# Optimization experiments

Measured on AMD Instinct MI355X. Metric: run time of the kernel, lower is better.

The kernel has to match this reference:

```python
import jax, jax.numpy as jnp
import numpy as np

N = 10000       # nodes (cells)
NFEAT = 2000    # gene-expression features
NFE = 256       # embed features
NH = 128        # nhid
NHE = 64        # nhid_embed
L = 2           # gcn_hid_layers_num
NOUT = 20       # output classes
BN_EPS = 1e-5


def bn_eval(x, g, b, rm, rv):
    # BatchNorm1d in eval mode: affine with running stats
    return g * (x - rm) / jnp.sqrt(rv + BN_EPS) + b


def lstm_layer(seq, Wih, Whh, bih, bhh):
    # seq: [T, N, H_in]; PyTorch gate order i, f, g, o
    Hd = Whh.shape[1]
    def step(carry, xt):
        h, c = carry
        z = xt @ Wih.T + h @ Whh.T + bih + bhh  # [N, 4H]
        i, f, g, o = jnp.split(z, 4, axis=1)
        c = jax.nn.sigmoid(f) * c + jax.nn.sigmoid(i) * jnp.tanh(g)
        h = jax.nn.sigmoid(o) * jnp.tanh(c)
        return (h, c), h
    h0 = jnp.zeros((seq.shape[1], Hd), seq.dtype)
    _, hs = jax.lax.scan(step, (h0, h0), seq)
    return hs  # [T, N, H]


def setup_inputs() -> dict:
    key = jax.random.key(0)
    ks = iter(jax.random.split(key, 48))
    def rn(shape, scale=1.0):
        return jax.random.normal(next(ks), shape, dtype=jnp.float32) * scale
    inp = {}
    inp["x"] = rn((N, NFEAT))
    inp["embed"] = rn((N, NFE))
    inp["adj"] = jax.random.uniform(next(ks), (N, N), dtype=jnp.float32)
    inp["W_in"] = rn((NH, NFEAT), NFEAT ** -0.5); inp["b_in"] = jnp.zeros((NH,), jnp.float32)
    inp["bn_in_g"] = jnp.ones((NH,), jnp.float32); inp["bn_in_b"] = jnp.zeros((NH,), jnp.float32)
    inp["bn_in_rm"] = rn((NH,), 0.1); inp["bn_in_rv"] = jnp.ones((NH,), jnp.float32)
    # gs_block: Linear(2*nhid -> nhid) per layer (concat self + mean-aggregated neighbors)
    inp["W_gs"] = rn((L, NH, 2 * NH), (2 * NH) ** -0.5); inp["b_gs"] = jnp.zeros((L, NH), jnp.float32)
    for l in range(2):  # 2-layer LSTM jumping-knowledge
        inp[f"Wih{l}"] = rn((4 * NH, NH), NH ** -0.5)
        inp[f"Whh{l}"] = rn((4 * NH, NH), NH ** -0.5)
        inp[f"bih{l}"] = jnp.zeros((4 * NH,), jnp.float32)
        inp[f"bhh{l}"] = jnp.zeros((4 * NH,), jnp.float32)
    inp["W_emb"] = rn((NHE, NFE), NFE ** -0.5); inp["b_emb"] = jnp.zeros((NHE,), jnp.float32)
    inp["bn_emb_g"] = jnp.ones((NHE,), jnp.float32); inp["bn_emb_b"] = jnp.zeros((NHE,), jnp.float32)
    inp["bn_emb_rm"] = rn((NHE,), 0.1); inp["bn_emb_rv"] = jnp.ones((NHE,), jnp.float32)
    D = NH + NHE
    inp["W_fc"] = rn((D, D), D ** -0.5); inp["b_fc"] = jnp.zeros((D,), jnp.float32)
    inp["bn_fc_g"] = jnp.ones((D,), jnp.float32); inp["bn_fc_b"] = jnp.zeros((D,), jnp.float32)
    inp["bn_fc_rm"] = rn((D,), 0.1); inp["bn_fc_rv"] = jnp.ones((D,), jnp.float32)
    inp["W_out"] = rn((NOUT, D), D ** -0.5); inp["b_out"] = jnp.zeros((NOUT,), jnp.float32)
    return inp


def _forward(x, embed, adj, W_in, b_in, bn_in_g, bn_in_b, bn_in_rm, bn_in_rv,
             W_gs, b_gs, Wih0, Whh0, bih0, bhh0, Wih1, Whh1, bih1, bhh1,
             W_emb, b_emb, bn_emb_g, bn_emb_b, bn_emb_rm, bn_emb_rv,
             W_fc, b_fc, bn_fc_g, bn_fc_b, bn_fc_rm, bn_fc_rv, W_out, b_out):
    # input projection + BN + ELU (dropout: eval mode -> no-op)
    h = jax.nn.elu(bn_eval(x @ W_in.T + b_in, bn_in_g, bn_in_b, bn_in_rm, bn_in_rv))
    # GraphSAGE mean aggregator: row-normalized dense adjacency
    adj_norm = adj / adj.sum(1, keepdims=True)
    jk = []
    for l in range(L):
        neigh = adj_norm @ h                              # [N, NH] neighbor mean
        comb = jnp.concatenate([h, neigh], axis=1)        # [N, 2NH] (gcn=False)
        h = jax.nn.relu(comb @ W_gs[l].T + b_gs[l])
        h = h / jnp.maximum(jnp.linalg.norm(h, axis=1, keepdims=True), 1e-12)  # F.normalize
        jk.append(h)
    seq = jnp.stack(jk, 0)                                # [L, N, NH]
    hs = lstm_layer(seq, Wih0, Whh0, bih0, bhh0)
    hs = lstm_layer(hs, Wih1, Whh1, bih1, bhh1)
    h = hs.mean(0)                                        # JK: mean of LSTM outputs
    h = jax.nn.elu(bn_eval(h, bn_in_g, bn_in_b, bn_in_rm, bn_in_rv))  # bn_node_in_exp reused
    e = jax.nn.elu(bn_eval(embed @ W_emb.T + b_emb, bn_emb_g, bn_emb_b, bn_emb_rm, bn_emb_rv))
    h = jnp.concatenate([h, e], axis=1)                   # [N, NH+NHE]
    h = jax.nn.elu(bn_eval(h @ W_fc.T + b_fc, bn_fc_g, bn_fc_b, bn_fc_rm, bn_fc_rv))
    logits = h @ W_out.T + b_out
    return jax.nn.log_softmax(logits, axis=1)


def reference(x, embed, adj, W_in, b_in, bn_in_g, bn_in_b, bn_in_rm, bn_in_rv,
              W_gs, b_gs, Wih0, Whh0, bih0, bhh0, Wih1, Whh1, bih1, bhh1,
              W_emb, b_emb, bn_emb_g, bn_emb_b, bn_emb_rm, bn_emb_rv,
              W_fc, b_fc, bn_fc_g, bn_fc_b, bn_fc_rm, bn_fc_rv, W_out, b_out):
    return _forward(x, embed, adj, W_in, b_in, bn_in_g, bn_in_b, bn_in_rm, bn_in_rv,
                    W_gs, b_gs, Wih0, Whh0, bih0, bhh0, Wih1, Whh1, bih1, bhh1,
                    W_emb, b_emb, bn_emb_g, bn_emb_b, bn_emb_rm, bn_emb_rv,
                    W_fc, b_fc, bn_fc_g, bn_fc_b, bn_fc_rm, bn_fc_rv, W_out, b_out)
```

## Files before the change

### kernel.cpp

```cpp
#include <hip/hip_runtime.h>
#include <hip/hip_bf16.h>
#include <math.h>

#define N_NODES 10000
#define NFEAT   2000
#define NFE     256
#define NH      128
#define NHE     64
#define NOUT    20
#define DCAT    192
#define BN_EPS  1e-5f

#define KP      10016
#define KSTEPS  313
#define MT      157
#define NSPLIT  16
#define KC      20
#define NSPLX   4
#define MPAD    10048

typedef __attribute__((ext_vector_type(8))) short  bf16x8;
typedef __attribute__((ext_vector_type(4))) float  f32x4;

__device__ __forceinline__ float sigm(float x) { return 1.0f / (1.0f + expf(-x)); }

__device__ __forceinline__ unsigned short f2bf(float x) {
    union { __hip_bfloat16 h; unsigned short u; } c;
    c.h = __float2bfloat16(x);
    return c.u;
}

__device__ __forceinline__ float bf2f(unsigned short u) {
    union { float f; unsigned int i; } c;
    c.i = ((unsigned int)u) << 16;
    return c.f;
}

__device__ __forceinline__ bf16x8 cvt8(const float* v) {
    bf16x8 r;
    #pragma unroll
    for (int i = 0; i < 8; ++i) r[i] = (short)f2bf(v[i]);
    return r;
}

__global__ __launch_bounds__(256) void wconv_kernel(const float* __restrict__ Wih0,
                                                    const float* __restrict__ Whh0,
                                                    const float* __restrict__ Wih1,
                                                    const float* __restrict__ Whh1,
                                                    const float* __restrict__ Wgs,
                                                    unsigned short* __restrict__ wl,
                                                    unsigned short* __restrict__ wgb)
{
    const int total = 262144 + 65536;
    for (int i = blockIdx.x * 256 + threadIdx.x; i < total; i += gridDim.x * 256) {
        if (i < 262144) {
            int l = i >> 17, rem = i & 131071;
            int n = rem >> 8, k = rem & 255;
            const float* src;
            if (l == 0) src = (k < 128) ? (Wih0 + n * 128 + k) : (Whh0 + n * 128 + (k - 128));
            else        src = (k < 128) ? (Wih1 + n * 128 + k) : (Whh1 + n * 128 + (k - 128));
            wl[i] = f2bf(*src);
        } else {
            int j = i - 262144;
            wgb[j] = f2bf(Wgs[j]);
        }
    }
}

__global__ __launch_bounds__(256) void adjmm_kernel(const float* __restrict__ adj,
                                                    const unsigned short* __restrict__ hT,
                                                    unsigned short* __restrict__ part,
                                                    float* __restrict__ part_s)
{
    __shared__ unsigned short sa[2][64 * 32];
    __shared__ unsigned short sb[2][128 * 32];
    const int tid  = threadIdx.x;
    const int lane = tid & 63, w = tid >> 6;
    const int m0   = blockIdx.x * 64;
    const int ks0  = blockIdx.y * KC;
    const int ks1  = min(ks0 + KC, KSTEPS);
    const int r0   = (w & 1) * 32;
    const int c0   = (w >> 1) * 64;

    const int arow = tid >> 2, agrp = tid & 3;
    const size_t abase = (size_t)min(m0 + arow, N_NODES - 1) * N_NODES;
    const int bcol = tid >> 1, bg0 = (tid & 1) * 2;

    const int asoff  = arow * 32 + ((agrp ^ (arow & 3)) << 3);
    const int bsoff0 = bcol * 32 + (((bg0 + 0) ^ (bcol & 3)) << 3);
    const int bsoff1 = bcol * 32 + (((bg0 + 1) ^ (bcol & 3)) << 3);

    float rs = 0.f;
    f32x4 acc[2][4];
    #pragma unroll
    for (int i = 0; i < 2; ++i)
        #pragma unroll
        for (int j = 0; j < 4; ++j) acc[i][j] = (f32x4){0.f, 0.f, 0.f, 0.f};

    float av8[8];
    bf16x8 vb0, vb1;
    auto load_step = [&](int ks) {
        const int k0 = ks * 32;
        const int kg = k0 + agrp * 8;
        if (kg + 8 <= N_NODES) {
            float4 u0 = *(const float4*)(adj + abase + kg);
            float4 u1 = *(const float4*)(adj + abase + kg + 4);
            av8[0] = u0.x; av8[1] = u0.y; av8[2] = u0.z; av8[3] = u0.w;
            av8[4] = u1.x; av8[5] = u1.y; av8[6] = u1.z; av8[7] = u1.w;
        } else {
            #pragma unroll
            for (int i = 0; i < 8; ++i) av8[i] = 0.f;
        }
        vb0 = *(const bf16x8*)(hT + (size_t)bcol * KP + k0 + bg0 * 8);
        vb1 = *(const bf16x8*)(hT + (size_t)bcol * KP + k0 + (bg0 + 1) * 8);
    };
    auto write_step = [&](int p) {
        #pragma unroll
        for (int i = 0; i < 8; ++i) rs += av8[i];
        *(bf16x8*)(sa[p] + asoff)  = cvt8(av8);
        *(bf16x8*)(sb[p] + bsoff0) = vb0;
        *(bf16x8*)(sb[p] + bsoff1) = vb1;
    };

    load_step(ks0);
    write_step(0);

    for (int ks = ks0; ks < ks1; ++ks) {
        const int p = (ks - ks0) & 1;
        const bool more = (ks + 1 < ks1);
        if (more) load_step(ks + 1);
        __syncthreads();
        bf16x8 av[2], bv[4];
        #pragma unroll
        for (int rb = 0; rb < 2; ++rb) {
            int row = r0 + rb * 16 + (lane & 15);
            int g   = lane >> 4;
            av[rb] = *(const bf16x8*)(sa[p] + row * 32 + ((g ^ (row & 3)) << 3));
        }
        #pragma unroll
        for (int cb = 0; cb < 4; ++cb) {
            int col = c0 + cb * 16 + (lane & 15);
            int g   = lane >> 4;
            bv[cb] = *(const bf16x8*)(sb[p] + col * 32 + ((g ^ (col & 3)) << 3));
        }
        #pragma unroll
        for (int rb = 0; rb < 2; ++rb)
            #pragma unroll
            for (int cb = 0; cb < 4; ++cb)
                acc[rb][cb] = __builtin_amdgcn_mfma_f32_16x16x32_bf16(av[rb], bv[cb],
                                                                      acc[rb][cb], 0, 0, 0);
        if (more) write_step(p ^ 1);
    }

    rs += __shfl_xor(rs, 1);
    rs += __shfl_xor(rs, 2);
    if ((tid & 3) == 0) part_s[(size_t)blockIdx.y * MPAD + m0 + arow] = rs;

    unsigned short* pout = part + (size_t)blockIdx.y * MPAD * NH;
    #pragma unroll
    for (int rb = 0; rb < 2; ++rb)
        #pragma unroll
        for (int cb = 0; cb < 4; ++cb) {
            int rowb = m0 + r0 + rb * 16 + (lane >> 4) * 4;
            int col  = c0 + cb * 16 + (lane & 15);
            #pragma unroll
            for (int reg = 0; reg < 4; ++reg)
                pout[(size_t)(rowb + reg) * NH + col] = f2bf(acc[rb][cb][reg]);
        }
}

__global__ __launch_bounds__(256) void xw_mfma_kernel(const float* __restrict__ x,
                                                      const float* __restrict__ Wn,
                                                      float* __restrict__ part)
{
    __shared__ unsigned short sa[2][64 * 32];
    __shared__ unsigned short sb[2][128 * 32];
    const int tid  = threadIdx.x;
    const int lane = tid & 63, w = tid >> 6;
    const int m0   = blockIdx.x * 64;
    const int TOT  = (NFEAT + 31) / 32;
    const int s0   = blockIdx.y * 16;
    const int s1   = min(s0 + 16, TOT);
    const int r0   = (w & 1) * 32;
    const int c0   = (w >> 1) * 64;

    const int arow = tid >> 2, agrp = tid & 3;
    const size_t abase = (size_t)min(m0 + arow, N_NODES - 1) * NFEAT;
    const int asoff = arow * 32 + ((agrp ^ (arow & 3)) << 3);
    int bn_[2], bgrp_[2], bsoff_[2];
    #pragma unroll
    for (int t = 0; t < 2; ++t) {
        int gi = tid + t * 256;
        bn_[t] = gi >> 2; bgrp_[t] = gi & 3;
        bsoff_[t] = bn_[t] * 32 + ((bgrp_[t] ^ (bn_[t] & 3)) << 3);
    }

    f32x4 acc[2][4];
    #pragma unroll
    for (int i = 0; i < 2; ++i)
        #pragma unroll
        for (int j = 0; j < 4; ++j) acc[i][j] = (f32x4){0.f, 0.f, 0.f, 0.f};

    float av8[8], bv8[2][8];
    auto load_step = [&](int ks) {
        const int k0 = ks * 32;
        {
            const int kg = k0 + agrp * 8;
            if (kg + 8 <= NFEAT) {
                float4 u0 = *(const float4*)(x + abase + kg);
                float4 u1 = *(const float4*)(x + abase + kg + 4);
                av8[0]=u0.x; av8[1]=u0.y; av8[2]=u0.z; av8[3]=u0.w;
                av8[4]=u1.x; av8[5]=u1.y; av8[6]=u1.z; av8[7]=u1.w;
            } else {
                #pragma unroll
                for (int i = 0; i < 8; ++i) av8[i] = 0.f;
            }
        }
        #pragma unroll
        for (int t = 0; t < 2; ++t) {
            int kg = k0 + bgrp_[t] * 8;
            if (kg + 8 <= NFEAT) {
                float4 u0 = *(const float4*)(Wn + (size_t)bn_[t] * NFEAT + kg);
                float4 u1 = *(const float4*)(Wn + (size_t)bn_[t] * NFEAT + kg + 4);
                bv8[t][0]=u0.x; bv8[t][1]=u0.y; bv8[t][2]=u0.z; bv8[t][3]=u0.w;
                bv8[t][4]=u1.x; bv8[t][5]=u1.y; bv8[t][6]=u1.z; bv8[t][7]=u1.w;
            } else {
                #pragma unroll
                for (int i = 0; i < 8; ++i) bv8[t][i] = 0.f;
            }
        }
    };
    auto write_step = [&](int p) {
        *(bf16x8*)(sa[p] + asoff) = cvt8(av8);
        #pragma unroll
        for (int t = 0; t < 2; ++t)
            *(bf16x8*)(sb[p] + bsoff_[t]) = cvt8(bv8[t]);
    };

    load_step(s0);
    write_step(0);

    for (int ks = s0; ks < s1; ++ks) {
        const int p = (ks - s0) & 1;
        const bool more = (ks + 1 < s1);
        if (more) load_step(ks + 1);
        __syncthreads();
        bf16x8 av[2], bv[4];
        #pragma unroll
        for (int rb = 0; rb < 2; ++rb) {
            int row = r0 + rb * 16 + (lane & 15);
            int g   = lane >> 4;
            av[rb] = *(const bf16x8*)(sa[p] + row * 32 + ((g ^ (row & 3)) << 3));
        }
        #pragma unroll
        for (int cb = 0; cb < 4; ++cb) {
            int col = c0 + cb * 16 + (lane & 15);
            int g   = lane >> 4;
            bv[cb] = *(const bf16x8*)(sb[p] + col * 32 + ((g ^ (col & 3)) << 3));
        }
        #pragma unroll
        for (int rb = 0; rb < 2; ++rb)
            #pragma unroll
            for (int cb = 0; cb < 4; ++cb)
                acc[rb][cb] = __builtin_amdgcn_mfma_f32_16x16x32_bf16(av[rb], bv[cb],
                                                                      acc[rb][cb], 0, 0, 0);
        if (more) write_step(p ^ 1);
    }
    float* pout = part + (size_t)blockIdx.y * MPAD * NH;
    #pragma unroll
    for (int rb = 0; rb < 2; ++rb)
        #pragma unroll
        for (int cb = 0; cb < 4; ++cb) {
            int rowb = m0 + r0 + rb * 16 + (lane >> 4) * 4;
            int col  = c0 + cb * 16 + (lane & 15);
            #pragma unroll
            for (int reg = 0; reg < 4; ++reg)
                pout[(size_t)(rowb + reg) * NH + col] = acc[rb][cb][reg];
        }
}

__global__ __launch_bounds__(256) void xw_reduce_kernel(const float* __restrict__ part,
                                                        const float* __restrict__ bias,
                                                        const float* __restrict__ g,
                                                        const float* __restrict__ bb,
                                                        const float* __restrict__ rm,
                                                        const float* __restrict__ rv,
                                                        float* __restrict__ h,
                                                        unsigned short* __restrict__ hT)
{
    __shared__ unsigned short tb[128][8];
    const int tid = threadIdx.x;
    int idx = blockIdx.x * 256 + tid;
    const int c4 = (tid & 31) * 4;
    const int lr = tid >> 5;
    const int m0g = blockIdx.x * 8;
    const size_t ch = (size_t)MPAD * NH / 4;
    const float4* p = (const float4*)part;
    float a[4] = {0.f, 0.f, 0.f, 0.f};
    #pragma unroll
    for (int c = 0; c < NSPLX; ++c) {
        float4 v = p[c * ch + idx];
        a[0] += v.x; a[1] += v.y; a[2] += v.z; a[3] += v.w;
    }
    float o[4];
    #pragma unroll
    for (int j = 0; j < 4; ++j) {
        int c = c4 + j;
        float sc = g[c] / sqrtf(rv[c] + BN_EPS);
        float t = (a[j] + bias[c] - rm[c]) * sc + bb[c];
        o[j] = t > 0.f ? t : expm1f(t);
        tb[c][lr] = f2bf(o[j]);
    }
    float4 ov; ov.x = o[0]; ov.y = o[1]; ov.z = o[2]; ov.w = o[3];
    *(float4*)(h + (size_t)idx * 4) = ov;
    __syncthreads();
    if (tid < 128) {
        ushort4 v0, v1;
        v0.x = tb[tid][0]; v0.y = tb[tid][1]; v0.z = tb[tid][2]; v0.w = tb[tid][3];
        v1.x = tb[tid][4]; v1.y = tb[tid][5]; v1.z = tb[tid][6]; v1.w = tb[tid][7];
        *(ushort4*)(hT + (size_t)tid * KP + m0g)     = v0;
        *(ushort4*)(hT + (size_t)tid * KP + m0g + 4) = v1;
        if (blockIdx.x == 0) {
            ushort4 zz; zz.x = zz.y = zz.z = zz.w = 0;
            #pragma unroll
            for (int q = 0; q < 4; ++q)
                *(ushort4*)(hT + (size_t)tid * KP + 10000 + q * 4) = zz;
        }
    }
}

template<bool WRITE_T>
__global__ __launch_bounds__(256) void gs_fused_kernel(const float* __restrict__ h,
                                                       const unsigned short* __restrict__ part,
                                                       const float* __restrict__ part_s,
                                                       const unsigned short* __restrict__ Wg,
                                                       const float* __restrict__ bg,
                                                       float* __restrict__ jk,
                                                       unsigned short* __restrict__ jkT)
{
    __shared__ unsigned short sa[64 * 32];
    __shared__ unsigned short sb[128 * 32];
    __shared__ float ssq_l[64][2];
    __shared__ unsigned short tb[WRITE_T ? 128 * 64 : 1];
    const int tid  = threadIdx.x;
    const int lane = tid & 63, w = tid >> 6;
    const int m0   = blockIdx.x * 64;
    const int r0   = (w & 1) * 32;
    const int c0   = (w >> 1) * 64;
    const int arow = tid >> 2, agrp = tid & 3;
    const int mg   = min(m0 + arow, N_NODES - 1);

    float inv;
    {
        float s = 0.f;
        #pragma unroll
        for (int c = 0; c < NSPLIT; ++c) s += part_s[(size_t)c * MPAD + mg];
        inv = 1.0f / s;
    }

    f32x4 acc[2][4];
    #pragma unroll
    for (int i = 0; i < 2; ++i)
        #pragma unroll
        for (int j = 0; j < 4; ++j) acc[i][j] = (f32x4){0.f, 0.f, 0.f, 0.f};

    for (int k0 = 0; k0 < 256; k0 += 32) {
        const int kg = k0 + agrp * 8;
        float a8[8];
        if (kg < 128) {
            const float* asrc = h + (size_t)mg * NH + kg;
            float4 u0 = *(const float4*)asrc;
            float4 u1 = *(const float4*)(asrc + 4);
            a8[0]=u0.x; a8[1]=u0.y; a8[2]=u0.z; a8[3]=u0.w;
            a8[4]=u1.x; a8[5]=u1.y; a8[6]=u1.z; a8[7]=u1.w;
        } else {
            const int cc = kg - 128;
            float s[8] = {0.f,0.f,0.f,0.f,0.f,0.f,0.f,0.f};
            #pragma unroll
            for (int c = 0; c < NSPLIT; ++c) {
                bf16x8 v = *(const bf16x8*)(part + (size_t)c * MPAD * NH + (size_t)mg * NH + cc);
                #pragma unroll
                for (int i = 0; i < 8; ++i) s[i] += bf2f((unsigned short)v[i]);
            }
            #pragma unroll
            for (int i = 0; i < 8; ++i) a8[i] = s[i] * inv;
        }
        bf16x8 b8[2];
        #pragma unroll
        for (int t = 0; t < 2; ++t) {
            int gi = tid + t * 256;
            int n = gi >> 2, grp = gi & 3;
            b8[t] = *(const bf16x8*)(Wg + (size_t)n * 256 + k0 + grp * 8);
        }
        __syncthreads();
        *(bf16x8*)(sa + arow * 32 + ((agrp ^ (arow & 3)) << 3)) = cvt8(a8);
        #pragma unroll
        for (int t = 0; t < 2; ++t) {
            int gi = tid + t * 256;
            int n = gi >> 2, grp = gi & 3;
            *(bf16x8*)(sb + n * 32 + ((grp ^ (n & 3)) << 3)) = b8[t];
        }
        __syncthreads();
        bf16x8 av[2], bv[4];
        #pragma unroll
        for (int rb = 0; rb < 2; ++rb) {
            int row = r0 + rb * 16 + (lane & 15);
            int g   = lane >> 4;
            av[rb] = *(const bf16x8*)(sa + row * 32 + ((g ^ (row & 3)) << 3));
        }
        #pragma unroll
        for (int cb = 0; cb < 4; ++cb) {
            int col = c0 + cb * 16 + (lane & 15);
            int g   = lane >> 4;
            bv[cb] = *(const bf16x8*)(sb + col * 32 + ((g ^ (col & 3)) << 3));
        }
        #pragma unroll
        for (int rb = 0; rb < 2; ++rb)
            #pragma unroll
            for (int cb = 0; cb < 4; ++cb)
                acc[rb][cb] = __builtin_amdgcn_mfma_f32_16x16x32_bf16(av[rb], bv[cb],
                                                                      acc[rb][cb], 0, 0, 0);
    }

    float vv[2][4][4];
    float ps[2][4] = {};
    #pragma unroll
    for (int rb = 0; rb < 2; ++rb)
        #pragma unroll
        for (int cb = 0; cb < 4; ++cb) {
            int colg = c0 + cb * 16 + (lane & 15);
            float b = bg[colg];
            #pragma unroll
            for (int reg = 0; reg < 4; ++reg) {
                float t = fmaxf(acc[rb][cb][reg] + b, 0.f);
                vv[rb][cb][reg] = t;
                ps[rb][reg] += t * t;
            }
        }
    #pragma unroll
    for (int msk = 1; msk < 16; msk <<= 1)
        #pragma unroll
        for (int rb = 0; rb < 2; ++rb)
            #pragma unroll
            for (int reg = 0; reg < 4; ++reg)
                ps[rb][reg] += __shfl_xor(ps[rb][reg], msk);
    if ((lane & 15) == 0) {
        #pragma unroll
        for (int rb = 0; rb < 2; ++rb)
            #pragma unroll
            for (int reg = 0; reg < 4; ++reg)
                ssq_l[r0 + rb * 16 + (lane >> 4) * 4 + reg][w >> 1] = ps[rb][reg];
    }
    __syncthreads();
    #pragma unroll
    for (int rb = 0; rb < 2; ++rb)
        #pragma unroll
        for (int reg = 0; reg < 4; ++reg) {
            int lr = r0 + rb * 16 + (lane >> 4) * 4 + reg;
            float s = ssq_l[lr][0] + ssq_l[lr][1];
            float sc = 1.0f / fmaxf(sqrtf(s), 1e-12f);
            int m = m0 + lr;
            #pragma unroll
            for (int cb = 0; cb < 4; ++cb) {
                int colg = c0 + cb * 16 + (lane & 15);
                float o = vv[rb][cb][reg] * sc;
                if (m < N_NODES) jk[(size_t)m * NH + colg] = o;
                if constexpr (WRITE_T) tb[colg * 64 + lr] = f2bf(o);
            }
        }
    if constexpr (WRITE_T) {
        __syncthreads();
        #pragma unroll
        for (int p = 0; p < 4; ++p) {
            int flat = (tid + p * 256) * 8;
            int c = flat >> 6, mo = flat & 63;
            int kglob = m0 + mo;
            if (kglob < KP) {
                unsigned short tmp[8];
                #pragma unroll
                for (int i = 0; i < 8; ++i)
                    tmp[i] = (kglob + i < N_NODES) ? tb[c * 64 + mo + i] : (unsigned short)0;
                ushort4 v0, v1;
                v0.x = tmp[0]; v0.y = tmp[1]; v0.z = tmp[2]; v0.w = tmp[3];
                v1.x = tmp[4]; v1.y = tmp[5]; v1.z = tmp[6]; v1.w = tmp[7];
                *(ushort4*)(jkT + (size_t)c * KP + kglob)     = v0;
                *(ushort4*)(jkT + (size_t)c * KP + kglob + 4) = v1;
            }
        }
    }
}

__global__ __launch_bounds__(256) void lstm4_kernel(
    const float* __restrict__ jk0, const float* __restrict__ jk1,
    const unsigned short* __restrict__ wl,
    const float* __restrict__ bih0, const float* __restrict__ bhh0,
    const float* __restrict__ bih1, const float* __restrict__ bhh1,
    const float* __restrict__ bng, const float* __restrict__ bnb,
    const float* __restrict__ bnrm, const float* __restrict__ bnrv,
    float* __restrict__ hpost)
{
    __shared__ unsigned short sa[32 * 32];
    __shared__ unsigned short sb[512 * 32];
    __shared__ unsigned short hb[2][32][136];
    const int tid = threadIdx.x, lane = tid & 63, w = tid >> 6;
    const int m0 = blockIdx.x * 32;
    const int arow = tid >> 2, agrp = tid & 3;
    const int mg = min(m0 + arow, N_NODES - 1);

    f32x4 acc[2][8];
    float cst[2][2][4];

    auto zacc = [&] {
        #pragma unroll
        for (int i = 0; i < 2; ++i)
            #pragma unroll
            for (int j = 0; j < 8; ++j) acc[i][j] = (f32x4){0.f, 0.f, 0.f, 0.f};
    };
    auto stage_sb = [&](const unsigned short* wlayer, int k0) {
        #pragma unroll
        for (int t = 0; t < 8; ++t) {
            int gi = tid + t * 256, n = gi >> 2, grp = gi & 3;
            *(bf16x8*)(sb + n * 32 + ((grp ^ (n & 3)) << 3)) =
                *(const bf16x8*)(wlayer + (size_t)n * 256 + k0 + grp * 8);
        }
    };
    auto stage_sa = [&](const float* a, int k0) {
        if (tid < 128) {
            int kg = k0 + agrp * 8;
            const float* src = a + (size_t)mg * NH + kg;
            float4 u0 = *(const float4*)src, u1 = *(const float4*)(src + 4);
            float a8[8] = {u0.x, u0.y, u0.z, u0.w, u1.x, u1.y, u1.z, u1.w};
            *(bf16x8*)(sa + arow * 32 + ((agrp ^ (arow & 3)) << 3)) = cvt8(a8);
        }
    };
    auto av_sa = [&](int rb) {
        int row = rb * 16 + (lane & 15), g = lane >> 4;
        return *(const bf16x8*)(sa + row * 32 + ((g ^ (row & 3)) << 3));
    };
    auto av_hb = [&](int i, int rb, int kl) {
        int row = rb * 16 + (lane & 15), g = lane >> 4;
        return *(const bf16x8*)(&hb[i][row][kl + g * 8]);
    };
    auto mfma_all = [&](bf16x8 a0, bf16x8 a1) {
        #pragma unroll
        for (int gate = 0; gate < 4; ++gate)
            #pragma unroll
            for (int cb = 0; cb < 2; ++cb) {
                int col = gate * 128 + w * 32 + cb * 16 + (lane & 15);
                int g = lane >> 4;
                bf16x8 bv = *(const bf16x8*)(sb + col * 32 + ((g ^ (col & 3)) << 3));
                acc[0][gate * 2 + cb] =
                    __builtin_amdgcn_mfma_f32_16x16x32_bf16(a0, bv, acc[0][gate * 2 + cb], 0, 0, 0);
                acc[1][gate * 2 + cb] =
                    __builtin_amdgcn_mfma_f32_16x16x32_bf16(a1, bv, acc[1][gate * 2 + cb], 0, 0, 0);
            }
    };
    auto epi = [&](const float* bih, const float* bhh, bool hasc, int hdst, bool fin) {
        __syncthreads();
        #pragma unroll
        for (int cb = 0; cb < 2; ++cb) {
            int cg = w * 32 + cb * 16 + (lane & 15);
            float bi  = bih[cg]       + bhh[cg];
            float bf_ = bih[128 + cg] + bhh[128 + cg];
            float bgg = bih[256 + cg] + bhh[256 + cg];
            float bo  = bih[384 + cg] + bhh[384 + cg];
            float sc = 0.f, sh = 0.f;
            if (fin) {
                sc = bng[cg] / sqrtf(bnrv[cg] + BN_EPS);
                sh = bnb[cg] - bnrm[cg] * sc;
            }
            #pragma unroll
            for (int rb = 0; rb < 2; ++rb)
                #pragma unroll
                for (int reg = 0; reg < 4; ++reg) {
                    int lr = rb * 16 + (lane >> 4) * 4 + reg;
                    float zi = acc[rb][0 + cb][reg] + bi;
                    float zf = acc[rb][2 + cb][reg] + bf_;
                    float zg = acc[rb][4 + cb][reg] + bgg;
                    float zo = acc[rb][6 + cb][reg] + bo;
                    float cn = sigm(zi) * tanhf(zg);
                    if (hasc) cn += sigm(zf) * cst[rb][cb][reg];
                    cst[rb][cb][reg] = cn;
                    float hv = sigm(zo) * tanhf(cn);
                    if (fin) {
                        float hm = bf2f(hb[0][lr][cg]);
                        float t = 0.5f * (hm + hv);
                        t = t * sc + sh;
                        int m = m0 + lr;
                        if (m < N_NODES) hpost[(size_t)m * NH + cg] = t > 0.f ? t : expm1f(t);
                    } else {
                        hb[hdst][lr][cg] = f2bf(hv);
                    }
                }
        }
        __syncthreads();
    };

    zacc();
    for (int k0 = 0; k0 < 128; k0 += 32) {
        __syncthreads();
        stage_sa(jk0, k0);
        stage_sb(wl, k0);
        __syncthreads();
        mfma_all(av_sa(0), av_sa(1));
    }
    epi(bih0, bhh0, false, 0, false);

    zacc();
    for (int k0 = 0; k0 < 256; k0 += 32) {
        __syncthreads();
        if (k0 < 128) stage_sa(jk1, k0);
        stage_sb(wl, k0);
        __syncthreads();
        if (k0 < 128) mfma_all(av_sa(0), av_sa(1));
        else          mfma_all(av_hb(0, 0, k0 - 128), av_hb(0, 1, k0 - 128));
    }
    epi(bih0, bhh0, true, 1, false);

    const unsigned short* wl1 = wl + 512 * 256;
    zacc();
    for (int k0 = 0; k0 < 128; k0 += 32) {
        __syncthreads();
        stage_sb(wl1, k0);
        __syncthreads();
        mfma_all(av_hb(0, 0, k0), av_hb(0, 1, k0));
    }
    epi(bih1, bhh1, false, 0, false);

    zacc();
    for (int k0 = 0; k0 < 256; k0 += 32) {
        __syncthreads();
        stage_sb(wl1, k0);
        __syncthreads();
        if (k0 < 128) mfma_all(av_hb(1, 0, k0), av_hb(1, 1, k0));
        else          mfma_all(av_hb(0, 0, k0 - 128), av_hb(0, 1, k0 - 128));
    }
    epi(bih1, bhh1, true, -1, true);
}

__global__ __launch_bounds__(256) void epilogue_kernel(
    const float* __restrict__ embed,
    const float* __restrict__ W_emb, const float* __restrict__ b_emb,
    const float* __restrict__ bn_e_g, const float* __restrict__ bn_e_b,
    const float* __restrict__ bn_e_rm, const float* __restrict__ bn_e_rv,
    const float* __restrict__ hpost,
    const float* __restrict__ W_fc, const float* __restrict__ b_fc,
    const float* __restrict__ bn_f_g, const float* __restrict__ bn_f_b,
    const float* __restrict__ bn_f_rm, const float* __restrict__ bn_f_rv,
    const float* __restrict__ W_out, const float* __restrict__ b_out,
    float* __restrict__ out)
{
    __shared__ unsigned short sa[64 * 32];
    __shared__ unsigned short sb[192 * 32];
    __shared__ unsigned short ebuf[64][72];
    __shared__ float fbuf[64][204];
    const int tid = threadIdx.x, lane = tid & 63, w = tid >> 6;
    const int m0 = blockIdx.x * 64;
    const int arow = tid >> 2, agrp = tid & 3;
    const int mg = min(m0 + arow, N_NODES - 1);
    const int g = lane >> 4;

    f32x4 aE[4];
    #pragma unroll
    for (int j = 0; j < 4; ++j) aE[j] = (f32x4){0.f, 0.f, 0.f, 0.f};
    for (int k0 = 0; k0 < NFE; k0 += 32) {
        float a8[8], b8[8];
        {
            const float* s = embed + (size_t)mg * NFE + k0 + agrp * 8;
            float4 u0 = *(const float4*)s, u1 = *(const float4*)(s + 4);
            a8[0]=u0.x; a8[1]=u0.y; a8[2]=u0.z; a8[3]=u0.w;
            a8[4]=u1.x; a8[5]=u1.y; a8[6]=u1.z; a8[7]=u1.w;
        }
        {
            const float* s = W_emb + (size_t)arow * NFE + k0 + agrp * 8;
            float4 u0 = *(const float4*)s, u1 = *(const float4*)(s + 4);
            b8[0]=u0.x; b8[1]=u0.y; b8[2]=u0.z; b8[3]=u0.w;
            b8[4]=u1.x; b8[5]=u1.y; b8[6]=u1.z; b8[7]=u1.w;
        }
        __syncthreads();
        *(bf16x8*)(sa + arow * 32 + ((agrp ^ (arow & 3)) << 3)) = cvt8(a8);
        *(bf16x8*)(sb + arow * 32 + ((agrp ^ (arow & 3)) << 3)) = cvt8(b8);
        __syncthreads();
        bf16x8 av;
        { int row = w * 16 + (lane & 15);
          av = *(const bf16x8*)(sa + row * 32 + ((g ^ (row & 3)) << 3)); }
        #pragma unroll
        for (int cb = 0; cb < 4; ++cb) {
            int col = cb * 16 + (lane & 15);
            bf16x8 bv = *(const bf16x8*)(sb + col * 32 + ((g ^ (col & 3)) << 3));
            aE[cb] = __builtin_amdgcn_mfma_f32_16x16x32_bf16(av, bv, aE[cb], 0, 0, 0);
        }
    }
    #pragma unroll
    for (int cb = 0; cb < 4; ++cb) {
        int col = cb * 16 + (lane & 15);
        float sc = bn_e_g[col] / sqrtf(bn_e_rv[col] + BN_EPS);
        float sh = bn_e_b[col] - bn_e_rm[col] * sc;
        float bb = b_emb[col];
        #pragma unroll
        for (int reg = 0; reg < 4; ++reg) {
            int row = w * 16 + (lane >> 4) * 4 + reg;
            float t = (aE[cb][reg] + bb) * sc + sh;
            ebuf[row][col] = f2bf(t > 0.f ? t : expm1f(t));
        }
    }
    __syncthreads();

    f32x4 aF[4][3];
    #pragma unroll
    for (int i = 0; i < 4; ++i)
        #pragma unroll
        for (int j = 0; j < 3; ++j) aF[i][j] = (f32x4){0.f, 0.f, 0.f, 0.f};
    for (int k0 = 0; k0 < DCAT; k0 += 32) {
        const bool gl = (k0 < 128);
        float b8[3][8];
        #pragma unroll
        for (int t = 0; t < 3; ++t) {
            int gi = tid + t * 256, n = gi >> 2, grp = gi & 3;
            const float* s = W_fc + (size_t)n * DCAT + k0 + grp * 8;
            float4 u0 = *(const float4*)s, u1 = *(const float4*)(s + 4);
            b8[t][0]=u0.x; b8[t][1]=u0.y; b8[t][2]=u0.z; b8[t][3]=u0.w;
            b8[t][4]=u1.x; b8[t][5]=u1.y; b8[t][6]=u1.z; b8[t][7]=u1.w;
        }
        float a8[8];
        if (gl) {
            const float* s = hpost + (size_t)mg * NH + k0 + agrp * 8;
            float4 u0 = *(const float4*)s, u1 = *(const float4*)(s + 4);
            a8[0]=u0.x; a8[1]=u0.y; a8[2]=u0.z; a8[3]=u0.w;
            a8[4]=u1.x; a8[5]=u1.y; a8[6]=u1.z; a8[7]=u1.w;
        }
        __syncthreads();
        if (gl) *(bf16x8*)(sa + arow * 32 + ((agrp ^ (arow & 3)) << 3)) = cvt8(a8);
        #pragma unroll
        for (int t = 0; t < 3; ++t) {
            int gi = tid + t * 256, n = gi >> 2, grp = gi & 3;
            *(bf16x8*)(sb + n * 32 + ((grp ^ (n & 3)) << 3)) = cvt8(b8[t]);
        }
        __syncthreads();
        #pragma unroll
        for (int rf = 0; rf < 4; ++rf) {
            int row = rf * 16 + (lane & 15);
            bf16x8 av = gl ? *(const bf16x8*)(sa + row * 32 + ((g ^ (row & 3)) << 3))
                           : *(const bf16x8*)(&ebuf[row][(k0 - 128) + g * 8]);
            #pragma unroll
            for (int cf = 0; cf < 3; ++cf) {
                int col = w * 48 + cf * 16 + (lane & 15);
                bf16x8 bv = *(const bf16x8*)(sb + col * 32 + ((g ^ (col & 3)) << 3));
                aF[rf][cf] = __builtin_amdgcn_mfma_f32_16x16x32_bf16(av, bv, aF[rf][cf], 0, 0, 0);
            }
        }
    }
    #pragma unroll
    for (int cf = 0; cf < 3; ++cf) {
        int col = w * 48 + cf * 16 + (lane & 15);
        float sc = bn_f_g[col] / sqrtf(bn_f_rv[col] + BN_EPS);
        float sh = bn_f_b[col] - bn_f_rm[col] * sc;
        float bb = b_fc[col];
        #pragma unroll
        for (int rf = 0; rf < 4; ++rf)
            #pragma unroll
            for (int reg = 0; reg < 4; ++reg) {
                int row = rf * 16 + (lane >> 4) * 4 + reg;
                float t = (aF[rf][cf][reg] + bb) * sc + sh;
                fbuf[row][col] = t > 0.f ? t : expm1f(t);
            }
    }
    __syncthreads();

    f32x4 aO[2];
    aO[0] = (f32x4){0.f, 0.f, 0.f, 0.f};
    aO[1] = (f32x4){0.f, 0.f, 0.f, 0.f};
    for (int k0 = 0; k0 < DCAT; k0 += 32) {
        float b8[8];
        const bool act = tid < 128;
        if (act) {
            if (arow < NOUT) {
                const float* s = W_out + (size_t)arow * DCAT + k0 + agrp * 8;
                float4 u0 = *(const float4*)s, u1 = *(const float4*)(s + 4);
                b8[0]=u0.x; b8[1]=u0.y; b8[2]=u0.z; b8[3]=u0.w;
                b8[4]=u1.x; b8[5]=u1.y; b8[6]=u1.z; b8[7]=u1.w;
            } else {
                #pragma unroll
                for (int i = 0; i < 8; ++i) b8[i] = 0.f;
            }
        }
        __syncthreads();
        if (act) *(bf16x8*)(sb + arow * 32 + ((agrp ^ (arow & 3)) << 3)) = cvt8(b8);
        __syncthreads();
        int row = w * 16 + (lane & 15);
        float4 f0 = *(const float4*)(&fbuf[row][k0 + g * 8]);
        float4 f1 = *(const float4*)(&fbuf[row][k0 + g * 8 + 4]);
        float f8[8] = {f0.x, f0.y, f0.z, f0.w, f1.x, f1.y, f1.z, f1.w};
        bf16x8 av = cvt8(f8);
        #pragma unroll
        for (int cf = 0; cf < 2; ++cf) {
            int col = cf * 16 + (lane & 15);
            bf16x8 bv = *(const bf16x8*)(sb + col * 32 + ((g ^ (col & 3)) << 3));
            aO[cf] = __builtin_amdgcn_mfma_f32_16x16x32_bf16(av, bv, aO[cf], 0, 0, 0);
        }
    }
    const int c0i = lane & 15, c1i = 16 + (lane & 15);
    const bool v1 = c1i < NOUT;
    #pragma unroll
    for (int reg = 0; reg < 4; ++reg) {
        int row = w * 16 + (lane >> 4) * 4 + reg;
        int m = m0 + row;
        float l0 = aO[0][reg] + b_out[c0i];
        float l1 = v1 ? (aO[1][reg] + b_out[c1i]) : -INFINITY;
        float mx = fmaxf(l0, l1);
        #pragma unroll
        for (int msk = 1; msk < 16; msk <<= 1) mx = fmaxf(mx, __shfl_xor(mx, msk));
        float s = expf(l0 - mx) + (v1 ? expf(l1 - mx) : 0.f);
        #pragma unroll
        for (int msk = 1; msk < 16; msk <<= 1) s += __shfl_xor(s, msk);
        float lse = mx + logf(s);
        if (m < N_NODES) {
            out[(size_t)m * NOUT + c0i] = l0 - lse;
            if (v1) out[(size_t)m * NOUT + c1i] = l1 - lse;
        }
    }
}

extern "C" void kernel_launch(void* const* d_in, const int* in_sizes, int n_in,
                              void* d_out, int out_size, void* d_ws, size_t ws_size,
                              hipStream_t stream)
{
    const float* x       = (const float*)d_in[0];
    const float* embed   = (const float*)d_in[1];
    const float* adj     = (const float*)d_in[2];
    const float* W_in    = (const float*)d_in[3];
    const float* b_in    = (const float*)d_in[4];
    const float* bn_in_g = (const float*)d_in[5];
    const float* bn_in_b = (const float*)d_in[6];
    const float* bn_in_rm= (const float*)d_in[7];
    const float* bn_in_rv= (const float*)d_in[8];
    const float* W_gs    = (const float*)d_in[9];
    const float* b_gs    = (const float*)d_in[10];
    const float* Wih0    = (const float*)d_in[11];
    const float* Whh0    = (const float*)d_in[12];
    const float* bih0    = (const float*)d_in[13];
    const float* bhh0    = (const float*)d_in[14];
    const float* Wih1    = (const float*)d_in[15];
    const float* Whh1    = (const float*)d_in[16];
    const float* bih1    = (const float*)d_in[17];
    const float* bhh1    = (const float*)d_in[18];
    const float* W_emb   = (const float*)d_in[19];
    const float* b_emb   = (const float*)d_in[20];
    const float* bn_e_g  = (const float*)d_in[21];
    const float* bn_e_b  = (const float*)d_in[22];
    const float* bn_e_rm = (const float*)d_in[23];
    const float* bn_e_rv = (const float*)d_in[24];
    const float* W_fc    = (const float*)d_in[25];
    const float* b_fc    = (const float*)d_in[26];
    const float* bn_f_g  = (const float*)d_in[27];
    const float* bn_f_b  = (const float*)d_in[28];
    const float* bn_f_rm = (const float*)d_in[29];
    const float* bn_f_rv = (const float*)d_in[30];
    const float* W_out   = (const float*)d_in[31];
    const float* b_out   = (const float*)d_in[32];
    float* outp = (float*)d_out;

    const size_t HB = (size_t)N_NODES * NH * sizeof(float);
    char* wp = (char*)d_ws;
    auto carve = [&](size_t bytes) {
        void* p = (void*)wp;
        wp += (bytes + 1023) & ~(size_t)1023;
        return p;
    };
    void* partRaw = carve((size_t)NSPLIT * MPAD * NH * 2);
    unsigned short* partB = (unsigned short*)partRaw;
    float* partF = (float*)partRaw;
    float* part_s= (float*)carve((size_t)NSPLIT * MPAD * sizeof(float));
    float* h_in  = (float*)carve(HB);
    float* jk0   = (float*)carve(HB);
    float* jk1   = (float*)carve(HB);
    float* hpost = (float*)carve(HB);
    unsigned short* hT  = (unsigned short*)carve((size_t)NH * KP * 2);
    unsigned short* wl  = (unsigned short*)carve((size_t)2 * 512 * 256 * 2);
    unsigned short* wgb = (unsigned short*)carve((size_t)2 * 128 * 256 * 2);
    if ((size_t)(wp - (char*)d_ws) > ws_size) return;

    const dim3 blk(256);

    wconv_kernel<<<320, blk, 0, stream>>>(Wih0, Whh0, Wih1, Whh1, W_gs, wl, wgb);

    xw_mfma_kernel<<<dim3(MT, NSPLX), blk, 0, stream>>>(x, W_in, partF);
    xw_reduce_kernel<<<1250, blk, 0, stream>>>(partF, b_in, bn_in_g, bn_in_b,
                                               bn_in_rm, bn_in_rv, h_in, hT);

    adjmm_kernel<<<dim3(MT, NSPLIT), blk, 0, stream>>>(adj, hT, partB, part_s);
    gs_fused_kernel<true><<<MT, blk, 0, stream>>>(h_in, partB, part_s, wgb, b_gs, jk0, hT);

    adjmm_kernel<<<dim3(MT, NSPLIT), blk, 0, stream>>>(adj, hT, partB, part_s);
    gs_fused_kernel<false><<<MT, blk, 0, stream>>>(jk0, partB, part_s, wgb + 128 * 256,
                                                   b_gs + 128, jk1, nullptr);

    lstm4_kernel<<<313, blk, 0, stream>>>(jk0, jk1, wl, bih0, bhh0, bih1, bhh1,
                                          bn_in_g, bn_in_b, bn_in_rm, bn_in_rv, hpost);

    epilogue_kernel<<<MT, blk, 0, stream>>>(embed, W_emb, b_emb,
                                            bn_e_g, bn_e_b, bn_e_rm, bn_e_rv,
                                            hpost, W_fc, b_fc,
                                            bn_f_g, bn_f_b, bn_f_rm, bn_f_rv,
                                            W_out, b_out, outp);
}
```

Before: 475.4 us.

## Reverse second adj pass order, stage partial stores via LDS, fold weight conversion

The second adjacency matmul now walks its blocks in reverse grid order, so the tail of the adj matrix still held in the large last-level cache from the first pass is read first. The adjmm epilogue stages bf16 partial outputs through shared memory and writes them as coalesced 16-byte vectors instead of scattered 2-byte stores. The separate weight-conversion kernel is removed and its work is done by the y==0 blocks of xw_mfma_kernel, saving one launch. This adds an extra barrier and LDS round trip in adjmm, and puts conversion work on the tail of some xw blocks.

```diff
diff --git a/kernel.cpp b/kernel.cpp
--- a/kernel.cpp
+++ b/kernel.cpp
@@ -43,30 +43,7 @@
     return r;
 }
 
-__global__ __launch_bounds__(256) void wconv_kernel(const float* __restrict__ Wih0,
-                                                    const float* __restrict__ Whh0,
-                                                    const float* __restrict__ Wih1,
-                                                    const float* __restrict__ Whh1,
-                                                    const float* __restrict__ Wgs,
-                                                    unsigned short* __restrict__ wl,
-                                                    unsigned short* __restrict__ wgb)
-{
-    const int total = 262144 + 65536;
-    for (int i = blockIdx.x * 256 + threadIdx.x; i < total; i += gridDim.x * 256) {
-        if (i < 262144) {
-            int l = i >> 17, rem = i & 131071;
-            int n = rem >> 8, k = rem & 255;
-            const float* src;
-            if (l == 0) src = (k < 128) ? (Wih0 + n * 128 + k) : (Whh0 + n * 128 + (k - 128));
-            else        src = (k < 128) ? (Wih1 + n * 128 + k) : (Whh1 + n * 128 + (k - 128));
-            wl[i] = f2bf(*src);
-        } else {
-            int j = i - 262144;
-            wgb[j] = f2bf(Wgs[j]);
-        }
-    }
-}
-
+template<int REV>
 __global__ __launch_bounds__(256) void adjmm_kernel(const float* __restrict__ adj,
                                                     const unsigned short* __restrict__ hT,
                                                     unsigned short* __restrict__ part,
@@ -76,8 +53,10 @@
     __shared__ unsigned short sb[2][128 * 32];
     const int tid  = threadIdx.x;
     const int lane = tid & 63, w = tid >> 6;
-    const int m0   = blockIdx.x * 64;
-    const int ks0  = blockIdx.y * KC;
+    const int bx   = REV ? (int)gridDim.x - 1 - (int)blockIdx.x : (int)blockIdx.x;
+    const int by   = REV ? (int)gridDim.y - 1 - (int)blockIdx.y : (int)blockIdx.y;
+    const int m0   = bx * 64;
+    const int ks0  = by * KC;
     const int ks1  = min(ks0 + KC, KSTEPS);
     const int r0   = (w & 1) * 32;
     const int c0   = (w >> 1) * 64;
@@ -154,24 +133,39 @@
 
     rs += __shfl_xor(rs, 1);
     rs += __shfl_xor(rs, 2);
-    if ((tid & 3) == 0) part_s[(size_t)blockIdx.y * MPAD + m0 + arow] = rs;
-
-    unsigned short* pout = part + (size_t)blockIdx.y * MPAD * NH;
+    if ((tid & 3) == 0) part_s[(size_t)by * MPAD + m0 + arow] = rs;
+
+    unsigned short* bounce = (unsigned short*)sb;
+    __syncthreads();
     #pragma unroll
     for (int rb = 0; rb < 2; ++rb)
         #pragma unroll
         for (int cb = 0; cb < 4; ++cb) {
-            int rowb = m0 + r0 + rb * 16 + (lane >> 4) * 4;
-            int col  = c0 + cb * 16 + (lane & 15);
+            int lrb = r0 + rb * 16 + (lane >> 4) * 4;
+            int col = c0 + cb * 16 + (lane & 15);
             #pragma unroll
             for (int reg = 0; reg < 4; ++reg)
-                pout[(size_t)(rowb + reg) * NH + col] = f2bf(acc[rb][cb][reg]);
-        }
+                bounce[(lrb + reg) * 128 + col] = f2bf(acc[rb][cb][reg]);
+        }
+    __syncthreads();
+    unsigned short* pout = part + (size_t)by * MPAD * NH + (size_t)m0 * NH;
+    #pragma unroll
+    for (int t = 0; t < 4; ++t) {
+        int flat = tid + t * 256;
+        *(bf16x8*)(pout + flat * 8) = *(const bf16x8*)(bounce + flat * 8);
+    }
 }
 
 __global__ __launch_bounds__(256) void xw_mfma_kernel(const float* __restrict__ x,
                                                       const float* __restrict__ Wn,
-                                                      float* __restrict__ part)
+                                                      float* __restrict__ part,
+                                                      const float* __restrict__ Wih0,
+                                                      const float* __restrict__ Whh0,
+                                                      const float* __restrict__ Wih1,
+                                                      const float* __restrict__ Whh1,
+                                                      const float* __restrict__ Wgs,
+                                                      unsigned short* __restrict__ wl,
+                                                      unsigned short* __restrict__ wgb)
 {
     __shared__ unsigned short sa[2][64 * 32];
     __shared__ unsigned short sb[2][128 * 32];
@@ -277,6 +271,23 @@
             for (int reg = 0; reg < 4; ++reg)
                 pout[(size_t)(rowb + reg) * NH + col] = acc[rb][cb][reg];
         }
+
+    if (blockIdx.y == 0) {
+        const int total = 262144 + 65536;
+        for (int i = blockIdx.x * 256 + tid; i < total; i += MT * 256) {
+            if (i < 262144) {
+                int l = i >> 17, rem = i & 131071;
+                int n = rem >> 8, k = rem & 255;
+                const float* src;
+                if (l == 0) src = (k < 128) ? (Wih0 + n * 128 + k) : (Whh0 + n * 128 + (k - 128));
+                else        src = (k < 128) ? (Wih1 + n * 128 + k) : (Whh1 + n * 128 + (k - 128));
+                wl[i] = f2bf(*src);
+            } else {
+                int j = i - 262144;
+                wgb[j] = f2bf(Wgs[j]);
+            }
+        }
+    }
 }
 
 __global__ __launch_bounds__(256) void xw_reduce_kernel(const float* __restrict__ part,
@@ -882,16 +893,16 @@
 
     const dim3 blk(256);
 
-    wconv_kernel<<<320, blk, 0, stream>>>(Wih0, Whh0, Wih1, Whh1, W_gs, wl, wgb);
-
-    xw_mfma_kernel<<<dim3(MT, NSPLX), blk, 0, stream>>>(x, W_in, partF);
+    xw_mfma_kernel<<<dim3(MT, NSPLX), blk, 0, stream>>>(x, W_in, partF,
+                                                        Wih0, Whh0, Wih1, Whh1, W_gs,
+                                                        wl, wgb);
     xw_reduce_kernel<<<1250, blk, 0, stream>>>(partF, b_in, bn_in_g, bn_in_b,
                                                bn_in_rm, bn_in_rv, h_in, hT);
 
-    adjmm_kernel<<<dim3(MT, NSPLIT), blk, 0, stream>>>(adj, hT, partB, part_s);
+    adjmm_kernel<0><<<dim3(MT, NSPLIT), blk, 0, stream>>>(adj, hT, partB, part_s);
     gs_fused_kernel<true><<<MT, blk, 0, stream>>>(h_in, partB, part_s, wgb, b_gs, jk0, hT);
 
-    adjmm_kernel<<<dim3(MT, NSPLIT), blk, 0, stream>>>(adj, hT, partB, part_s);
+    adjmm_kernel<1><<<dim3(MT, NSPLIT), blk, 0, stream>>>(adj, hT, partB, part_s);
     gs_fused_kernel<false><<<MT, blk, 0, stream>>>(jk0, partB, part_s, wgb + 128 * 256,
                                                    b_gs + 128, jk1, nullptr);
 
```

Result: faster. 447.5 us (median of 2 runs) (-5.9%).
